# Optimization experiments

Hardware: AMD Instinct MI355X
Metric: run time of the kernel (lower is better)

## Reference

```python
import jax, jax.numpy as jnp
import numpy as np

B, N, NPOINT, NSAMPLE = 8, 4096, 1024, 32
IN_CH = 29
MLP = [64, 64, 128]
D_IN = IN_CH + 3  # 32
D_OUT = 128
EPS = 1e-5


def setup_inputs() -> dict:
    key = jax.random.key(0)
    ks = jax.random.split(key, 32)
    inp = {}
    inp["xyz"] = jax.random.normal(ks[0], (B, 3, N), jnp.float32)
    inp["points"] = jax.random.normal(ks[1], (B, IN_CH, N), jnp.float32)
    last = IN_CH + 3
    for i, oc in enumerate(MLP):
        inp[f"mlp_w{i}"] = jax.random.normal(ks[2 + i], (oc, last), jnp.float32) * np.sqrt(2.0 / last).astype(np.float32)
        inp[f"mlp_b{i}"] = jnp.zeros((oc,), jnp.float32)
        inp[f"mlp_g{i}"] = jnp.ones((oc,), jnp.float32)
        inp[f"mlp_be{i}"] = jnp.zeros((oc,), jnp.float32)
        last = oc
    inp["conv1_w"] = jax.random.normal(ks[10], (D_OUT // 2, 4), jnp.float32) * np.float32(np.sqrt(2.0 / 4))
    inp["conv1_b"] = jnp.zeros((D_OUT // 2,), jnp.float32)
    inp["bn1_g"] = jnp.ones((D_OUT // 2,), jnp.float32)
    inp["bn1_be"] = jnp.zeros((D_OUT // 2,), jnp.float32)
    inp["conv2_w"] = jax.random.normal(ks[11], (D_OUT // 2, D_IN), jnp.float32) * np.float32(np.sqrt(2.0 / D_IN))
    inp["conv2_b"] = jnp.zeros((D_OUT // 2,), jnp.float32)
    inp["bn2_g"] = jnp.ones((D_OUT // 2,), jnp.float32)
    inp["bn2_be"] = jnp.zeros((D_OUT // 2,), jnp.float32)
    return inp


def _conv1x1(x, w, b):
    # x: [B,Cin,ns,S], w: [Cout,Cin] -> [B,Cout,ns,S]
    return jnp.einsum("bcns,oc->bons", x, w) + b[None, :, None, None]


def _bn_relu(x, g, be):
    # training-mode BatchNorm2d: batch stats over (B, ns, S), biased variance
    m = jnp.mean(x, axis=(0, 2, 3), keepdims=True)
    v = jnp.var(x, axis=(0, 2, 3), keepdims=True)
    y = g[None, :, None, None] * (x - m) * jax.lax.rsqrt(v + EPS) + be[None, :, None, None]
    return jax.nn.relu(y)


def _fps(xyz):
    # xyz: [B,N,3] -> centroid indices [B,NPOINT]; deterministic start at index 0
    Bn, Nn, _ = xyz.shape

    def step(carry, _):
        dist, far = carry
        cen = jnp.take_along_axis(xyz, far[:, None, None], axis=1)  # [B,1,3]
        d = jnp.sum((xyz - cen) ** 2, axis=-1)                      # [B,N]
        dist = jnp.minimum(dist, d)
        new_far = jnp.argmax(dist, axis=-1).astype(jnp.int32)
        return (dist, new_far), far

    init = (jnp.full((Bn, Nn), 1e10, xyz.dtype), jnp.zeros((Bn,), jnp.int32))
    _, cents = jax.lax.scan(step, init, None, length=NPOINT)
    return cents.T  # [B,NPOINT]


def _forward(xyz, points, mlp_params, conv1_w, conv1_b, bn1_g, bn1_be,
             conv2_w, conv2_b, bn2_g, bn2_be):
    xyz_t = xyz.transpose(0, 2, 1)      # [B,N,3]
    pts_t = points.transpose(0, 2, 1)   # [B,N,C]
    xyz_sg = jax.lax.stop_gradient(xyz_t)

    ct_idx = _fps(xyz_sg)                                   # [B,S]
    bidx = jnp.arange(B)[:, None]
    ct_xyz = xyz_t[bidx, ct_idx]                            # [B,S,3]

    # kNN via squared distances (indices only -> stop_gradient)
    ct_sg = jax.lax.stop_gradient(ct_xyz)
    d2 = (jnp.sum(ct_sg ** 2, -1)[:, :, None]
          + jnp.sum(xyz_sg ** 2, -1)[:, None, :]
          - 2.0 * jnp.einsum("bsc,bnc->bsn", ct_sg, xyz_sg))  # [B,S,N]
    _, gidx = jax.lax.top_k(-d2, NSAMPLE)                     # [B,S,ns]

    bidx3 = jnp.arange(B)[:, None, None]
    grouped_xyz = xyz_t[bidx3, gidx]                          # [B,S,ns,3]
    ft_xyz = grouped_xyz - ct_xyz[:, :, None, :]              # [B,S,ns,3]
    ft_points = jnp.concatenate([ft_xyz, pts_t[bidx3, gidx]], axis=-1)  # [B,S,ns,3+C]
    ft = ft_points.transpose(0, 3, 2, 1)                      # [B,3+C,ns,S]

    # shared MLP (conv-bn-relu stack), then max over neighbors
    x = ft
    for (w, b, g, be) in mlp_params:
        x = _bn_relu(_conv1x1(x, w, b), g, be)
    new_points1 = jnp.max(x, axis=2)                          # [B,mlp[-1],S]

    # relative positional encoding branch
    ct_p = ct_xyz.transpose(0, 2, 1)                          # [B,3,S]
    grouped_p = grouped_xyz.transpose(0, 3, 2, 1)             # [B,3,ns,S]
    rel = grouped_p - ct_p[:, :, None, :]                     # [B,3,ns,S]
    rd = jnp.sqrt(jnp.maximum(jnp.sum(rel ** 2, axis=1, keepdims=True), 1e-12))
    new_xyz = _bn_relu(_conv1x1(jnp.concatenate([rel, rd], axis=1), conv1_w, conv1_b), bn1_g, bn1_be)
    new_pts = _bn_relu(_conv1x1(ft, conv2_w, conv2_b), bn2_g, bn2_be)

    f_concat = jnp.concatenate([new_xyz, new_pts], axis=1)    # [B,d_out,ns,S]
    new_points2 = jnp.concatenate([jnp.mean(f_concat, axis=2), jnp.max(f_concat, axis=2)], axis=1)
    conv_points = jnp.concatenate([new_points1, new_points2], axis=1)  # [B,mlp[-1]+2*d_out,S]
    return ct_p, conv_points


def reference(xyz, points,
              mlp_w0, mlp_b0, mlp_g0, mlp_be0,
              mlp_w1, mlp_b1, mlp_g1, mlp_be1,
              mlp_w2, mlp_b2, mlp_g2, mlp_be2,
              conv1_w, conv1_b, bn1_g, bn1_be,
              conv2_w, conv2_b, bn2_g, bn2_be):
    mlp_params = [(mlp_w0, mlp_b0, mlp_g0, mlp_be0),
                  (mlp_w1, mlp_b1, mlp_g1, mlp_be1),
                  (mlp_w2, mlp_b2, mlp_g2, mlp_be2)]
    return _forward(xyz, points, mlp_params, conv1_w, conv1_b, bn1_g, bn1_be,
                    conv2_w, conv2_b, bn2_g, bn2_be)
```

## Files before the change

kernel.cpp:

```cpp
#include <hip/hip_runtime.h>
#include <cfloat>
#include <math.h>

constexpr int B_ = 8, N_ = 4096, S_ = 1024, NS_ = 32;
constexpr int R_ = B_ * S_ * NS_;
constexpr float EPS_ = 1e-5f;

typedef float v2f __attribute__((ext_vector_type(2)));

__device__ __forceinline__ unsigned dpp_red_umax(unsigned x) {
    unsigned t;
#define STEP_(ctrl) t = (unsigned)__builtin_amdgcn_update_dpp((int)x, (int)x, ctrl, 0xf, 0xf, false); x = x > t ? x : t;
    STEP_(0x111) STEP_(0x112) STEP_(0x114) STEP_(0x118) STEP_(0x142) STEP_(0x143)
#undef STEP_
    return x;
}
__device__ __forceinline__ unsigned dpp_red_umin(unsigned x) {
    unsigned t;
#define STEP_(ctrl) t = (unsigned)__builtin_amdgcn_update_dpp((int)x, (int)x, ctrl, 0xf, 0xf, false); x = x < t ? x : t;
    STEP_(0x111) STEP_(0x112) STEP_(0x114) STEP_(0x118) STEP_(0x142) STEP_(0x143)
#undef STEP_
    return x;
}
__device__ __forceinline__ void dpp_min_u64(unsigned& hi, unsigned& lo) {
#define STEP_(ctrl) { \
    unsigned h2 = (unsigned)__builtin_amdgcn_update_dpp((int)hi, (int)hi, ctrl, 0xf, 0xf, false); \
    unsigned l2 = (unsigned)__builtin_amdgcn_update_dpp((int)lo, (int)lo, ctrl, 0xf, 0xf, false); \
    if (h2 < hi || (h2 == hi && l2 < lo)) { hi = h2; lo = l2; } }
    STEP_(0x111) STEP_(0x112) STEP_(0x114) STEP_(0x118) STEP_(0x142) STEP_(0x143)
#undef STEP_
}
__device__ __forceinline__ float dpp_sum_f32(float x) {
#define ADD_(ctrl, rm) { \
    int t_ = __builtin_amdgcn_update_dpp(0, __float_as_int(x), ctrl, rm, 0xf, true); \
    x += __int_as_float(t_); }
    ADD_(0x111, 0xf) ADD_(0x112, 0xf) ADD_(0x114, 0xf) ADD_(0x118, 0xf)
    ADD_(0x142, 0xa) ADD_(0x143, 0xc)
#undef ADD_
    return x;
}

__global__ __launch_bounds__(256) void transpose_kernel(const float* __restrict__ xyz,
                                                        const float* __restrict__ pts,
                                                        float* __restrict__ ptsT) {
    int idx = blockIdx.x * 256 + threadIdx.x;
    int b = idx >> 12, n = idx & (N_ - 1);
    float* row = ptsT + (size_t)idx * 32;
    const float* pb = pts + (size_t)b * 29 * N_;
#pragma unroll
    for (int c = 0; c < 29; c++) row[c] = pb[(size_t)c * N_ + n];
    const float* xb = xyz + (size_t)b * 3 * N_;
    row[29] = xb[n];
    row[30] = xb[N_ + n];
    row[31] = xb[2 * N_ + n];
}

__global__ __launch_bounds__(256) void fps_kernel(const float* __restrict__ xyz,
                                                  int* __restrict__ ct_idx) {
    int b = blockIdx.x;
    const float* xb = xyz + (size_t)b * 3 * N_;
    int t = threadIdx.x;
    __shared__ float sx[N_], sy[N_], sz[N_];
    __shared__ unsigned long long sb[2][4];
    for (int i = t; i < N_; i += 256) {
        sx[i] = xb[i];
        sy[i] = xb[N_ + i];
        sz[i] = xb[2 * N_ + i];
    }
    v2f px[8], py[8], pz[8], dist[8];
#pragma unroll
    for (int k = 0; k < 8; k++) {
        int n0 = (2 * k) * 256 + t, n1 = (2 * k + 1) * 256 + t;
        px[k] = (v2f){xb[n0], xb[n1]};
        py[k] = (v2f){xb[N_ + n0], xb[N_ + n1]};
        pz[k] = (v2f){xb[2 * N_ + n0], xb[2 * N_ + n1]};
        dist[k] = (v2f){1e10f, 1e10f};
    }
    __syncthreads();
    float cx = sx[0], cy = sy[0], cz = sz[0];
    int far = 0;
    int w = t >> 6;
    for (int it = 0; it < S_; it++) {
        if (t == 0) ct_idx[b * S_ + it] = far;
        v2f cx2 = (v2f){cx, cx}, cy2 = (v2f){cy, cy}, cz2 = (v2f){cz, cz};
#pragma unroll
        for (int k = 0; k < 8; k++) {
            v2f dx = px[k] - cx2, dy = py[k] - cy2, dz = pz[k] - cz2;
            v2f d = dx * dx;
            d = __builtin_elementwise_fma(dy, dy, d);
            d = __builtin_elementwise_fma(dz, dz, d);
            dist[k] = __builtin_elementwise_min(dist[k], d);
        }
        v2f m4[4];
#pragma unroll
        for (int k = 0; k < 4; k++)
            m4[k] = __builtin_elementwise_max(dist[2 * k], dist[2 * k + 1]);
        v2f m2a = __builtin_elementwise_max(m4[0], m4[1]);
        v2f m2b = __builtin_elementwise_max(m4[2], m4[3]);
        v2f m1 = __builtin_elementwise_max(m2a, m2b);
        float lmax = fmaxf(m1.x, m1.y);
        unsigned wm = (unsigned)__builtin_amdgcn_readlane(
            (int)dpp_red_umax(__float_as_uint(lmax)), 63);
        unsigned c8[8], c4i[4];
#pragma unroll
        for (int k = 0; k < 8; k++) {
            unsigned a = (__float_as_uint(dist[k].x) == wm)
                             ? (unsigned)((2 * k) * 256 + t) : 0xffffffffu;
            unsigned bq = (__float_as_uint(dist[k].y) == wm)
                             ? (unsigned)((2 * k + 1) * 256 + t) : 0xffffffffu;
            c8[k] = a < bq ? a : bq;
        }
#pragma unroll
        for (int k = 0; k < 4; k++) c4i[k] = c8[2 * k] < c8[2 * k + 1] ? c8[2 * k] : c8[2 * k + 1];
        unsigned c01 = c4i[0] < c4i[1] ? c4i[0] : c4i[1];
        unsigned c23 = c4i[2] < c4i[3] ? c4i[2] : c4i[3];
        unsigned mn = dpp_red_umin(c01 < c23 ? c01 : c23);
        int p = it & 1;
        if ((t & 63) == 63)
            sb[p][w] = ((unsigned long long)wm << 32) | (unsigned)~mn;
        __syncthreads();
        unsigned long long b0 = sb[p][0], b1 = sb[p][1], b2 = sb[p][2], b3 = sb[p][3];
        unsigned long long ma = b0 > b1 ? b0 : b1;
        unsigned long long mb = b2 > b3 ? b2 : b3;
        unsigned long long bw = ma > mb ? ma : mb;
        far = (int)(~(unsigned)(bw & 0xffffffffu)) & (N_ - 1);
        cx = sx[far]; cy = sy[far]; cz = sz[far];
    }
}

__global__ __launch_bounds__(256) void knn_kernel(const float* __restrict__ xyz,
                                                  const int* __restrict__ ct_idx,
                                                  int* __restrict__ gidx) {
    int bs = blockIdx.x;
    int b = bs >> 10;
    const float* xb = xyz + (size_t)b * 3 * N_;
    int ci = ct_idx[bs];
    float cx = xb[ci], cy = xb[N_ + ci], cz = xb[2 * N_ + ci];
    float cs = cx * cx + cy * cy + cz * cz;
    int t = threadIdx.x;
    unsigned long long pk[16];
#pragma unroll
    for (int j = 0; j < 16; j++) {
        int n = j * 256 + t;
        float x = xb[n], y = xb[N_ + n], z = xb[2 * N_ + n];
        float xn = x * x + y * y + z * z;
        float dot = cx * x + cy * y + cz * z;
        float val = cs + xn - 2.f * dot;
        unsigned vb = __float_as_uint(val);
        unsigned key = (vb & 0x80000000u) ? ~vb : (vb | 0x80000000u);
        pk[j] = ((unsigned long long)key << 32) | (unsigned)n;
    }
    __shared__ unsigned long long sw[2][4];
    int out_base = bs * NS_;
    int w = t >> 6;
    for (int iter = 0; iter < NS_; iter++) {
        unsigned long long m8[8], m4[4];
#pragma unroll
        for (int j = 0; j < 8; j++) m8[j] = pk[2 * j] < pk[2 * j + 1] ? pk[2 * j] : pk[2 * j + 1];
#pragma unroll
        for (int j = 0; j < 4; j++) m4[j] = m8[2 * j] < m8[2 * j + 1] ? m8[2 * j] : m8[2 * j + 1];
        unsigned long long ma = m4[0] < m4[1] ? m4[0] : m4[1];
        unsigned long long mb = m4[2] < m4[3] ? m4[2] : m4[3];
        unsigned long long best = ma < mb ? ma : mb;
        unsigned hi = (unsigned)(best >> 32), lo = (unsigned)best;
        dpp_min_u64(hi, lo);
        int p = iter & 1;
        if ((t & 63) == 63) sw[p][w] = ((unsigned long long)hi << 32) | lo;
        __syncthreads();
        unsigned long long b0 = sw[p][0], b1 = sw[p][1], b2 = sw[p][2], b3 = sw[p][3];
        unsigned long long wa = b0 < b1 ? b0 : b1;
        unsigned long long wb = b2 < b3 ? b2 : b3;
        unsigned long long bw = wa < wb ? wa : wb;
        int n = (int)(unsigned)(bw & 0xffffffffu);
        if (t == 0) gidx[out_base + iter] = n;
        if ((n & 255) == t) pk[n >> 8] = 0xFFFFFFFF00000000ull | (unsigned)n;
    }
}

__global__ __launch_bounds__(256) void gather_kernel(const float* __restrict__ ptsT,
                                                     const float* __restrict__ xyz,
                                                     const int* __restrict__ ct_idx,
                                                     const int* __restrict__ gidx,
                                                     float* __restrict__ ft,
                                                     float* __restrict__ out) {
    int r = blockIdx.x * 256 + threadIdx.x;
    int b = r >> 15;
    int s = (r >> 5) & (S_ - 1);
    int g = gidx[r];
    int ci = ct_idx[b * S_ + s];
    const float4* rowg = (const float4*)(ptsT + ((size_t)(b << 12) + g) * 32);
    float4 v[8];
#pragma unroll
    for (int i = 0; i < 8; i++) v[i] = rowg[i];
    float4 cw = ((const float4*)(ptsT + ((size_t)(b << 12) + ci) * 32))[7];
    float rx = v[7].y - cw.y;
    float ry = v[7].z - cw.z;
    float rz = v[7].w - cw.w;
    ft[r] = rx;
    ft[(size_t)R_ + r] = ry;
    ft[(size_t)2 * R_ + r] = rz;
    float rd = sqrtf(fmaxf(rx * rx + ry * ry + rz * rz, 1e-12f));
    ft[(size_t)32 * R_ + r] = rd;
    const float vals[32] = {v[0].x, v[0].y, v[0].z, v[0].w, v[1].x, v[1].y, v[1].z, v[1].w,
                            v[2].x, v[2].y, v[2].z, v[2].w, v[3].x, v[3].y, v[3].z, v[3].w,
                            v[4].x, v[4].y, v[4].z, v[4].w, v[5].x, v[5].y, v[5].z, v[5].w,
                            v[6].x, v[6].y, v[6].z, v[6].w, v[7].x, 0.f, 0.f, 0.f};
#pragma unroll
    for (int c = 0; c < 29; c++) ft[(size_t)(3 + c) * R_ + r] = vals[c];
    if (r < B_ * 3 * S_) {
        int bb = r / (3 * S_);
        int rem = r - bb * 3 * S_;
        int cc = rem >> 10;
        int ss = rem & (S_ - 1);
        int cidx = ct_idx[bb * S_ + ss];
        out[r] = xyz[(size_t)bb * 3 * N_ + (size_t)cc * N_ + cidx];
    }
}

template <int CIN, bool PRO>
__global__ __launch_bounds__(256) void convk(const float* __restrict__ xin,
                                             const float* __restrict__ W,
                                             const float* __restrict__ bias,
                                             const float* __restrict__ pread,
                                             const float* __restrict__ g,
                                             const float* __restrict__ be,
                                             float* __restrict__ pwrite, int pofs,
                                             float* __restrict__ out0,
                                             float* __restrict__ out1) {
    __shared__ float Ws[CIN][64];
    __shared__ float bs_[64];
    __shared__ float as_[CIN], bbs[CIN];
    __shared__ float red[4][64][2];
    int oc0 = blockIdx.y * 64;
    for (int i = threadIdx.x; i < CIN * 64; i += 256) {
        int o = i & 63, c = i >> 6;
        Ws[c][o] = W[(size_t)(oc0 + o) * CIN + c];
    }
    if (threadIdx.x < 64) bs_[threadIdx.x] = bias[oc0 + threadIdx.x];
    if (PRO) {
        int c = threadIdx.x >> 2, sub = threadIdx.x & 3;
        const float* ps = pread + (size_t)c * 1024 + sub * 128;
        float s = 0.f, q = 0.f;
        for (int i = 0; i < 128; i++) { s += ps[i]; q += ps[512 + i]; }
        s += __shfl_xor(s, 1); s += __shfl_xor(s, 2);
        q += __shfl_xor(q, 1); q += __shfl_xor(q, 2);
        if (sub == 0) {
            float inv = 1.0f / (float)R_;
            float mean = s * inv;
            float var = q * inv - mean * mean;
            float a = g[c] / sqrtf(var + EPS_);
            as_[c] = a;
            bbs[c] = be[c] - mean * a;
        }
    }
    __syncthreads();
    size_t r0 = (size_t)blockIdx.x * 512 + threadIdx.x;
    float acc0[64], acc1[64];
#pragma unroll
    for (int o = 0; o < 64; o++) { acc0[o] = 0.f; acc1[o] = 0.f; }
    for (int c = 0; c < CIN; c++) {
        float x0 = xin[(size_t)c * R_ + r0];
        float x1 = xin[(size_t)c * R_ + r0 + 256];
        if (PRO) {
            float a = as_[c], bb = bbs[c];
            x0 = fmaxf(fmaf(a, x0, bb), 0.f);
            x1 = fmaxf(fmaf(a, x1, bb), 0.f);
        }
#pragma unroll
        for (int o = 0; o < 64; o++) {
            float w = Ws[c][o];
            acc0[o] = fmaf(x0, w, acc0[o]);
            acc1[o] = fmaf(x1, w, acc1[o]);
        }
    }
    float* outp = blockIdx.y ? out1 : out0;
    int wv = threadIdx.x >> 6;
#pragma unroll
    for (int o = 0; o < 64; o++) {
        float bv = bs_[o];
        float y0 = acc0[o] + bv;
        float y1 = acc1[o] + bv;
        outp[(size_t)o * R_ + r0] = y0;
        outp[(size_t)o * R_ + r0 + 256] = y1;
        float s = y0 + y1;
        float q = fmaf(y0, y0, y1 * y1);
        s = dpp_sum_f32(s);
        q = dpp_sum_f32(q);
        if ((threadIdx.x & 63) == 63) { red[wv][o][0] = s; red[wv][o][1] = q; }
    }
    __syncthreads();
    if (threadIdx.x < 64) {
        int o = threadIdx.x;
        float s = red[0][o][0] + red[1][o][0] + red[2][o][0] + red[3][o][0];
        float q = red[0][o][1] + red[1][o][1] + red[2][o][1] + red[3][o][1];
        pwrite[(size_t)(pofs + oc0 + o) * 1024 + blockIdx.x] = s;
        pwrite[(size_t)(pofs + oc0 + o) * 1024 + 512 + blockIdx.x] = q;
    }
}

__global__ __launch_bounds__(256) void conv1_kernel(const float* __restrict__ ft,
                                                    const float* __restrict__ W,
                                                    const float* __restrict__ bias,
                                                    float* __restrict__ out,
                                                    float* __restrict__ pwrite, int pofs) {
    __shared__ float Ws[4][64];
    __shared__ float bs_[64];
    __shared__ float red[4][64][2];
    {
        int i = threadIdx.x;
        if (i < 256) { int o = i & 63, c = i >> 6; Ws[c][o] = W[o * 4 + c]; }
    }
    if (threadIdx.x < 64) bs_[threadIdx.x] = bias[threadIdx.x];
    __syncthreads();
    size_t r0 = (size_t)blockIdx.x * 512 + threadIdx.x;
    float acc0[64], acc1[64];
#pragma unroll
    for (int o = 0; o < 64; o++) { acc0[o] = 0.f; acc1[o] = 0.f; }
    const int chs[4] = {0, 1, 2, 32};
#pragma unroll
    for (int c = 0; c < 4; c++) {
        int ch = chs[c];
        float x0 = ft[(size_t)ch * R_ + r0];
        float x1 = ft[(size_t)ch * R_ + r0 + 256];
#pragma unroll
        for (int o = 0; o < 64; o++) {
            float w = Ws[c][o];
            acc0[o] = fmaf(x0, w, acc0[o]);
            acc1[o] = fmaf(x1, w, acc1[o]);
        }
    }
    int wv = threadIdx.x >> 6;
#pragma unroll
    for (int o = 0; o < 64; o++) {
        float bv = bs_[o];
        float y0 = acc0[o] + bv;
        float y1 = acc1[o] + bv;
        out[(size_t)o * R_ + r0] = y0;
        out[(size_t)o * R_ + r0 + 256] = y1;
        float s = y0 + y1;
        float q = fmaf(y0, y0, y1 * y1);
        s = dpp_sum_f32(s);
        q = dpp_sum_f32(q);
        if ((threadIdx.x & 63) == 63) { red[wv][o][0] = s; red[wv][o][1] = q; }
    }
    __syncthreads();
    if (threadIdx.x < 64) {
        int o = threadIdx.x;
        float s = red[0][o][0] + red[1][o][0] + red[2][o][0] + red[3][o][0];
        float q = red[0][o][1] + red[1][o][1] + red[2][o][1] + red[3][o][1];
        pwrite[(size_t)(pofs + o) * 1024 + blockIdx.x] = s;
        pwrite[(size_t)(pofs + o) * 1024 + 512 + blockIdx.x] = q;
    }
}

__global__ __launch_bounds__(64) void statsf(const float* __restrict__ partial,
                                             const float* __restrict__ g,
                                             const float* __restrict__ be,
                                             float* __restrict__ ab, int C) {
    int c = blockIdx.x, t = threadIdx.x;
    float s = 0.f, q = 0.f;
    for (int i = t; i < 512; i += 64) {
        s += partial[(size_t)c * 1024 + i];
        q += partial[(size_t)c * 1024 + 512 + i];
    }
    s = dpp_sum_f32(s);
    q = dpp_sum_f32(q);
    if (t == 63) {
        float inv = 1.0f / (float)R_;
        float mean = s * inv;
        float var = q * inv - mean * mean;
        float a = g[c] / sqrtf(var + EPS_);
        ab[c] = a;
        ab[C + c] = be[c] - mean * a;
    }
}

__global__ __launch_bounds__(64) void statsf2(const float* __restrict__ partial,
                                              const float* __restrict__ g1,
                                              const float* __restrict__ be1,
                                              const float* __restrict__ g2,
                                              const float* __restrict__ be2,
                                              float* __restrict__ ab) {
    int c = blockIdx.x, t = threadIdx.x;
    float s = 0.f, q = 0.f;
    for (int i = t; i < 512; i += 64) {
        s += partial[(size_t)c * 1024 + i];
        q += partial[(size_t)c * 1024 + 512 + i];
    }
    s = dpp_sum_f32(s);
    q = dpp_sum_f32(q);
    if (t == 63) {
        float gv = c < 64 ? g1[c] : g2[c - 64];
        float bv = c < 64 ? be1[c] : be2[c - 64];
        float inv = 1.0f / (float)R_;
        float mean = s * inv;
        float var = q * inv - mean * mean;
        float a = gv / sqrtf(var + EPS_);
        ab[c] = a;
        ab[128 + c] = bv - mean * a;
    }
}

__global__ __launch_bounds__(128) void final_max(const float* __restrict__ yA,
                                                 const float* __restrict__ yC,
                                                 const float* __restrict__ ab,
                                                 float* __restrict__ out) {
    int bs = blockIdx.x;
    int c = threadIdx.x;
    const float* src = (c < 64 ? yA + (size_t)c * R_ : yC + (size_t)(c - 64) * R_) + (size_t)bs * NS_;
    float a = ab[c], bb = ab[128 + c];
    const float4* s4 = reinterpret_cast<const float4*>(src);
    float m = -FLT_MAX;
#pragma unroll
    for (int i = 0; i < 8; i++) {
        float4 v = s4[i];
        m = fmaxf(m, fmaxf(fmaf(a, v.x, bb), 0.f));
        m = fmaxf(m, fmaxf(fmaf(a, v.y, bb), 0.f));
        m = fmaxf(m, fmaxf(fmaf(a, v.z, bb), 0.f));
        m = fmaxf(m, fmaxf(fmaf(a, v.w, bb), 0.f));
    }
    int b = bs >> 10, s = bs & (S_ - 1);
    out[24576 + (size_t)b * 393216 + (size_t)c * 1024 + s] = m;
}

__global__ __launch_bounds__(128) void final_meanmax(const float* __restrict__ z1,
                                                     const float* __restrict__ z2,
                                                     const float* __restrict__ ab,
                                                     float* __restrict__ out) {
    int bs = blockIdx.x;
    int c = threadIdx.x;
    const float* src = (c < 64 ? z1 + (size_t)c * R_ : z2 + (size_t)(c - 64) * R_) + (size_t)bs * NS_;
    float a = ab[c], bb = ab[128 + c];
    const float4* s4 = reinterpret_cast<const float4*>(src);
    float m = -FLT_MAX, sm = 0.f;
#pragma unroll
    for (int i = 0; i < 8; i++) {
        float4 v = s4[i];
        float t0 = fmaxf(fmaf(a, v.x, bb), 0.f); sm += t0; m = fmaxf(m, t0);
        float t1 = fmaxf(fmaf(a, v.y, bb), 0.f); sm += t1; m = fmaxf(m, t1);
        float t2 = fmaxf(fmaf(a, v.z, bb), 0.f); sm += t2; m = fmaxf(m, t2);
        float t3 = fmaxf(fmaf(a, v.w, bb), 0.f); sm += t3; m = fmaxf(m, t3);
    }
    int b = bs >> 10, s = bs & (S_ - 1);
    size_t ob = 24576 + (size_t)b * 393216;
    out[ob + (size_t)(128 + c) * 1024 + s] = sm * 0.03125f;
    out[ob + (size_t)(256 + c) * 1024 + s] = m;
}

extern "C" void kernel_launch(void* const* d_in, const int* in_sizes, int n_in,
                              void* d_out, int out_size, void* d_ws, size_t ws_size,
                              hipStream_t stream) {
    const float* xyz = (const float*)d_in[0];
    const float* pts = (const float*)d_in[1];
    const float* W0 = (const float*)d_in[2];  const float* b0 = (const float*)d_in[3];
    const float* g0 = (const float*)d_in[4];  const float* be0 = (const float*)d_in[5];
    const float* W1 = (const float*)d_in[6];  const float* b1 = (const float*)d_in[7];
    const float* g1 = (const float*)d_in[8];  const float* be1 = (const float*)d_in[9];
    const float* W2 = (const float*)d_in[10]; const float* b2 = (const float*)d_in[11];
    const float* g2 = (const float*)d_in[12]; const float* be2 = (const float*)d_in[13];
    const float* c1w = (const float*)d_in[14]; const float* c1b = (const float*)d_in[15];
    const float* bg1 = (const float*)d_in[16]; const float* bbe1 = (const float*)d_in[17];
    const float* c2w = (const float*)d_in[18]; const float* c2b = (const float*)d_in[19];
    const float* bg2 = (const float*)d_in[20]; const float* bbe2 = (const float*)d_in[21];
    float* out = (float*)d_out;

    int* ct_idx = (int*)d_ws;
    int* gidx = ct_idx + B_ * S_;
    float* fbase = (float*)d_ws;
    float* ft = fbase + 270336;
    float* A = ft + (size_t)33 * R_;
    float* Bb = A + (size_t)64 * R_;
    float* C = Bb + (size_t)64 * R_;
    float* pbufA = C + (size_t)64 * R_;
    float* pbufB = pbufA + 131072;
    float* ab2 = pbufB + 131072;
    float* abz = ab2 + 256;
    float* ptsT = A;

    transpose_kernel<<<B_ * N_ / 256, 256, 0, stream>>>(xyz, pts, ptsT);
    fps_kernel<<<B_, 256, 0, stream>>>(xyz, ct_idx);
    knn_kernel<<<B_ * S_, 256, 0, stream>>>(xyz, ct_idx, gidx);
    gather_kernel<<<R_ / 256, 256, 0, stream>>>(ptsT, xyz, ct_idx, gidx, ft, out);

    convk<32, false><<<dim3(R_ / 512, 1), 256, 0, stream>>>(ft, W0, b0, nullptr, nullptr, nullptr, pbufA, 0, A, nullptr);
    convk<64, true><<<dim3(R_ / 512, 1), 256, 0, stream>>>(A, W1, b1, pbufA, g0, be0, pbufB, 0, Bb, nullptr);
    convk<64, true><<<dim3(R_ / 512, 2), 256, 0, stream>>>(Bb, W2, b2, pbufB, g1, be1, pbufA, 0, A, C);
    statsf<<<128, 64, 0, stream>>>(pbufA, g2, be2, ab2, 128);
    final_max<<<B_ * S_, 128, 0, stream>>>(A, C, ab2, out);

    convk<32, false><<<dim3(R_ / 512, 1), 256, 0, stream>>>(ft, c2w, c2b, nullptr, nullptr, nullptr, pbufB, 64, Bb, nullptr);
    conv1_kernel<<<R_ / 512, 256, 0, stream>>>(ft, c1w, c1b, A, pbufB, 0);
    statsf2<<<128, 64, 0, stream>>>(pbufB, bg1, bbe1, bg2, bbe2, abz);
    final_meanmax<<<B_ * S_, 128, 0, stream>>>(A, Bb, abz, out);
}
```

Measured before the change: 1.355 ms.

## Restructure kNN to per-wave top-k merge, widen FPS, fold transpose into kNN

The kNN kernel now has each wave find its own 32 nearest candidates over a contiguous 1024-point slice without block barriers. One wave then merges the 128 candidates in a second pass, which removes 32 __syncthreads per block. FPS moves to 512 threads per batch, so each thread holds fewer points and there are eight wave partials to combine. The transpose becomes extra blocks appended to the kNN launch, dropping one launch and letting it overlap with kNN work. The cost is more per-wave selection work (each wave does 32 iterations of its own) and more cross-wave combining in FPS.

```diff
diff --git a/kernel.cpp b/kernel.cpp
--- a/kernel.cpp
+++ b/kernel.cpp
@@ -40,37 +40,22 @@
     return x;
 }
 
-__global__ __launch_bounds__(256) void transpose_kernel(const float* __restrict__ xyz,
-                                                        const float* __restrict__ pts,
-                                                        float* __restrict__ ptsT) {
-    int idx = blockIdx.x * 256 + threadIdx.x;
-    int b = idx >> 12, n = idx & (N_ - 1);
-    float* row = ptsT + (size_t)idx * 32;
-    const float* pb = pts + (size_t)b * 29 * N_;
-#pragma unroll
-    for (int c = 0; c < 29; c++) row[c] = pb[(size_t)c * N_ + n];
-    const float* xb = xyz + (size_t)b * 3 * N_;
-    row[29] = xb[n];
-    row[30] = xb[N_ + n];
-    row[31] = xb[2 * N_ + n];
-}
-
-__global__ __launch_bounds__(256) void fps_kernel(const float* __restrict__ xyz,
+__global__ __launch_bounds__(512) void fps_kernel(const float* __restrict__ xyz,
                                                   int* __restrict__ ct_idx) {
     int b = blockIdx.x;
     const float* xb = xyz + (size_t)b * 3 * N_;
     int t = threadIdx.x;
     __shared__ float sx[N_], sy[N_], sz[N_];
-    __shared__ unsigned long long sb[2][4];
-    for (int i = t; i < N_; i += 256) {
+    __shared__ unsigned long long sb[2][8];
+    for (int i = t; i < N_; i += 512) {
         sx[i] = xb[i];
         sy[i] = xb[N_ + i];
         sz[i] = xb[2 * N_ + i];
     }
-    v2f px[8], py[8], pz[8], dist[8];
-#pragma unroll
-    for (int k = 0; k < 8; k++) {
-        int n0 = (2 * k) * 256 + t, n1 = (2 * k + 1) * 256 + t;
+    v2f px[4], py[4], pz[4], dist[4];
+#pragma unroll
+    for (int k = 0; k < 4; k++) {
+        int n0 = (2 * k) * 512 + t, n1 = (2 * k + 1) * 512 + t;
         px[k] = (v2f){xb[n0], xb[n1]};
         py[k] = (v2f){xb[N_ + n0], xb[N_ + n1]};
         pz[k] = (v2f){xb[2 * N_ + n0], xb[2 * N_ + n1]};
@@ -84,34 +69,28 @@
         if (t == 0) ct_idx[b * S_ + it] = far;
         v2f cx2 = (v2f){cx, cx}, cy2 = (v2f){cy, cy}, cz2 = (v2f){cz, cz};
 #pragma unroll
-        for (int k = 0; k < 8; k++) {
+        for (int k = 0; k < 4; k++) {
             v2f dx = px[k] - cx2, dy = py[k] - cy2, dz = pz[k] - cz2;
             v2f d = dx * dx;
             d = __builtin_elementwise_fma(dy, dy, d);
             d = __builtin_elementwise_fma(dz, dz, d);
             dist[k] = __builtin_elementwise_min(dist[k], d);
         }
-        v2f m4[4];
-#pragma unroll
-        for (int k = 0; k < 4; k++)
-            m4[k] = __builtin_elementwise_max(dist[2 * k], dist[2 * k + 1]);
-        v2f m2a = __builtin_elementwise_max(m4[0], m4[1]);
-        v2f m2b = __builtin_elementwise_max(m4[2], m4[3]);
+        v2f m2a = __builtin_elementwise_max(dist[0], dist[1]);
+        v2f m2b = __builtin_elementwise_max(dist[2], dist[3]);
         v2f m1 = __builtin_elementwise_max(m2a, m2b);
         float lmax = fmaxf(m1.x, m1.y);
         unsigned wm = (unsigned)__builtin_amdgcn_readlane(
             (int)dpp_red_umax(__float_as_uint(lmax)), 63);
-        unsigned c8[8], c4i[4];
-#pragma unroll
-        for (int k = 0; k < 8; k++) {
+        unsigned c4i[4];
+#pragma unroll
+        for (int k = 0; k < 4; k++) {
             unsigned a = (__float_as_uint(dist[k].x) == wm)
-                             ? (unsigned)((2 * k) * 256 + t) : 0xffffffffu;
+                             ? (unsigned)((2 * k) * 512 + t) : 0xffffffffu;
             unsigned bq = (__float_as_uint(dist[k].y) == wm)
-                             ? (unsigned)((2 * k + 1) * 256 + t) : 0xffffffffu;
-            c8[k] = a < bq ? a : bq;
+                             ? (unsigned)((2 * k + 1) * 512 + t) : 0xffffffffu;
+            c4i[k] = a < bq ? a : bq;
         }
-#pragma unroll
-        for (int k = 0; k < 4; k++) c4i[k] = c8[2 * k] < c8[2 * k + 1] ? c8[2 * k] : c8[2 * k + 1];
         unsigned c01 = c4i[0] < c4i[1] ? c4i[0] : c4i[1];
         unsigned c23 = c4i[2] < c4i[3] ? c4i[2] : c4i[3];
         unsigned mn = dpp_red_umin(c01 < c23 ? c01 : c23);
@@ -120,17 +99,37 @@
             sb[p][w] = ((unsigned long long)wm << 32) | (unsigned)~mn;
         __syncthreads();
         unsigned long long b0 = sb[p][0], b1 = sb[p][1], b2 = sb[p][2], b3 = sb[p][3];
+        unsigned long long b4 = sb[p][4], b5 = sb[p][5], b6 = sb[p][6], b7 = sb[p][7];
         unsigned long long ma = b0 > b1 ? b0 : b1;
         unsigned long long mb = b2 > b3 ? b2 : b3;
-        unsigned long long bw = ma > mb ? ma : mb;
+        unsigned long long mc = b4 > b5 ? b4 : b5;
+        unsigned long long md = b6 > b7 ? b6 : b7;
+        unsigned long long me = ma > mb ? ma : mb;
+        unsigned long long mf = mc > md ? mc : md;
+        unsigned long long bw = me > mf ? me : mf;
         far = (int)(~(unsigned)(bw & 0xffffffffu)) & (N_ - 1);
         cx = sx[far]; cy = sy[far]; cz = sz[far];
     }
 }
 
 __global__ __launch_bounds__(256) void knn_kernel(const float* __restrict__ xyz,
+                                                  const float* __restrict__ pts,
                                                   const int* __restrict__ ct_idx,
-                                                  int* __restrict__ gidx) {
+                                                  int* __restrict__ gidx,
+                                                  float* __restrict__ ptsT) {
+    if (blockIdx.x >= 8192) {
+        int idx = (blockIdx.x - 8192) * 256 + threadIdx.x;
+        int b = idx >> 12, n = idx & (N_ - 1);
+        float* row = ptsT + (size_t)idx * 32;
+        const float* pb = pts + (size_t)b * 29 * N_;
+#pragma unroll
+        for (int c = 0; c < 29; c++) row[c] = pb[(size_t)c * N_ + n];
+        const float* xb = xyz + (size_t)b * 3 * N_;
+        row[29] = xb[n];
+        row[30] = xb[N_ + n];
+        row[31] = xb[2 * N_ + n];
+        return;
+    }
     int bs = blockIdx.x;
     int b = bs >> 10;
     const float* xb = xyz + (size_t)b * 3 * N_;
@@ -138,10 +137,11 @@
     float cx = xb[ci], cy = xb[N_ + ci], cz = xb[2 * N_ + ci];
     float cs = cx * cx + cy * cy + cz * cz;
     int t = threadIdx.x;
+    int w = t >> 6, lane = t & 63;
     unsigned long long pk[16];
 #pragma unroll
     for (int j = 0; j < 16; j++) {
-        int n = j * 256 + t;
+        int n = w * 1024 + j * 64 + lane;
         float x = xb[n], y = xb[N_ + n], z = xb[2 * N_ + n];
         float xn = x * x + y * y + z * z;
         float dot = cx * x + cy * y + cz * z;
@@ -150,9 +150,7 @@
         unsigned key = (vb & 0x80000000u) ? ~vb : (vb | 0x80000000u);
         pk[j] = ((unsigned long long)key << 32) | (unsigned)n;
     }
-    __shared__ unsigned long long sw[2][4];
-    int out_base = bs * NS_;
-    int w = t >> 6;
+    __shared__ unsigned long long cand[128];
     for (int iter = 0; iter < NS_; iter++) {
         unsigned long long m8[8], m4[4];
 #pragma unroll
@@ -164,16 +162,27 @@
         unsigned long long best = ma < mb ? ma : mb;
         unsigned hi = (unsigned)(best >> 32), lo = (unsigned)best;
         dpp_min_u64(hi, lo);
-        int p = iter & 1;
-        if ((t & 63) == 63) sw[p][w] = ((unsigned long long)hi << 32) | lo;
-        __syncthreads();
-        unsigned long long b0 = sw[p][0], b1 = sw[p][1], b2 = sw[p][2], b3 = sw[p][3];
-        unsigned long long wa = b0 < b1 ? b0 : b1;
-        unsigned long long wb = b2 < b3 ? b2 : b3;
-        unsigned long long bw = wa < wb ? wa : wb;
-        int n = (int)(unsigned)(bw & 0xffffffffu);
-        if (t == 0) gidx[out_base + iter] = n;
-        if ((n & 255) == t) pk[n >> 8] = 0xFFFFFFFF00000000ull | (unsigned)n;
+        unsigned whi = (unsigned)__builtin_amdgcn_readlane((int)hi, 63);
+        unsigned wlo = (unsigned)__builtin_amdgcn_readlane((int)lo, 63);
+        unsigned long long w64 = ((unsigned long long)whi << 32) | wlo;
+        if (lane == 63) cand[w * NS_ + iter] = w64;
+#pragma unroll
+        for (int j = 0; j < 16; j++)
+            pk[j] = (pk[j] == w64) ? 0xFFFFFFFFFFFFFFFFull : pk[j];
+    }
+    __syncthreads();
+    unsigned long long c0 = cand[2 * lane], c1 = cand[2 * lane + 1];
+    int out_base = bs * NS_;
+    for (int iter = 0; iter < NS_; iter++) {
+        unsigned long long mm = c0 < c1 ? c0 : c1;
+        unsigned hi = (unsigned)(mm >> 32), lo = (unsigned)mm;
+        dpp_min_u64(hi, lo);
+        unsigned whi = (unsigned)__builtin_amdgcn_readlane((int)hi, 63);
+        unsigned wlo = (unsigned)__builtin_amdgcn_readlane((int)lo, 63);
+        unsigned long long w64 = ((unsigned long long)whi << 32) | wlo;
+        if (t == 0) gidx[out_base + iter] = (int)wlo;
+        c0 = (c0 == w64) ? 0xFFFFFFFFFFFFFFFFull : c0;
+        c1 = (c1 == w64) ? 0xFFFFFFFFFFFFFFFFull : c1;
     }
 }
 
@@ -477,9 +486,8 @@
     float* abz = ab2 + 256;
     float* ptsT = A;
 
-    transpose_kernel<<<B_ * N_ / 256, 256, 0, stream>>>(xyz, pts, ptsT);
-    fps_kernel<<<B_, 256, 0, stream>>>(xyz, ct_idx);
-    knn_kernel<<<B_ * S_, 256, 0, stream>>>(xyz, ct_idx, gidx);
+    fps_kernel<<<B_, 512, 0, stream>>>(xyz, ct_idx);
+    knn_kernel<<<B_ * S_ + 128, 256, 0, stream>>>(xyz, pts, ct_idx, gidx, ptsT);
     gather_kernel<<<R_ / 256, 256, 0, stream>>>(ptsT, xyz, ct_idx, gidx, ft, out);
 
     convk<32, false><<<dim3(R_ / 512, 1), 256, 0, stream>>>(ft, W0, b0, nullptr, nullptr, nullptr, pbufA, 0, A, nullptr);
```

Measured after the change: 1.466 ms. 8.1% more time.
